# Performance work log

Hardware: AMD Instinct MI355X
Metric: run time of the kernel (lower is better)

## Reference

```python
import jax, jax.numpy as jnp
import numpy as np

N_NODES = 50000
N_EDGES = 800000
N_GRAPHS = 500
IN_DIM, HID, OUT = 128, 64, 10


def setup_inputs() -> dict:
    key = jax.random.key(0)
    ks = jax.random.split(key, 12)
    x = jax.random.normal(ks[0], (N_NODES, IN_DIM), dtype=jnp.float32)
    edge_index = jax.random.randint(ks[1], (2, N_EDGES), 0, N_NODES, dtype=jnp.int32)
    batch = jnp.sort(jax.random.randint(ks[2], (N_NODES,), 0, N_GRAPHS, dtype=jnp.int32))
    def glorot(k, shape):
        lim = np.sqrt(6.0 / (shape[0] + shape[1]))
        return jax.random.uniform(k, shape, jnp.float32, -lim, lim)
    return {
        "x": x, "edge_index": edge_index, "batch": batch,
        "W1": glorot(ks[3], (IN_DIM, HID)), "b1": jnp.zeros((HID,), jnp.float32),
        "W2": glorot(ks[4], (HID, HID)),    "b2": jnp.zeros((HID,), jnp.float32),
        "W3": glorot(ks[5], (HID, HID)),    "b3": jnp.zeros((HID,), jnp.float32),
        "lin_W1": glorot(ks[6], (HID, HID)), "lin_b1": jnp.zeros((HID,), jnp.float32),
        "lin_W2": glorot(ks[7], (HID, OUT)), "lin_b2": jnp.zeros((OUT,), jnp.float32),
    }


def _gcn_conv(x, src, dst, deg_inv_sqrt, W, b):
    # PyG GCNConv: h = x @ W, then sym-normalized scatter-add over edges (self-loops included in src/dst)
    h = x @ W                                   # [N, out]
    norm = deg_inv_sqrt[src] * deg_inv_sqrt[dst]  # [E+N]
    msgs = h[src] * norm[:, None]               # [E+N, out]  (large gathered intermediate)
    out = jax.ops.segment_sum(msgs, dst, num_segments=N_NODES)
    return out + b


def reference(x, edge_index, batch, W1, b1, W2, b2, W3, b3, lin_W1, lin_b1, lin_W2, lin_b2):
    # add self-loops once; degree (with edge weight 1) computed on target nodes
    loops = jnp.arange(N_NODES, dtype=edge_index.dtype)
    src = jnp.concatenate([edge_index[0], loops])
    dst = jnp.concatenate([edge_index[1], loops])
    deg = jax.ops.segment_sum(jnp.ones_like(dst, dtype=x.dtype), dst, num_segments=N_NODES)
    deg_inv_sqrt = jnp.where(deg > 0, jax.lax.rsqrt(jnp.maximum(deg, 1e-12)), 0.0)

    h = jax.nn.relu(_gcn_conv(x, src, dst, deg_inv_sqrt, W1, b1))
    h = jax.nn.relu(_gcn_conv(h, src, dst, deg_inv_sqrt, W2, b2))
    h = jax.nn.relu(_gcn_conv(h, src, dst, deg_inv_sqrt, W3, b3))

    # global mean pool over graphs
    sums = jax.ops.segment_sum(h, batch, num_segments=N_GRAPHS)
    counts = jax.ops.segment_sum(jnp.ones((h.shape[0],), h.dtype), batch, num_segments=N_GRAPHS)
    pooled = sums / jnp.maximum(counts, 1.0)[:, None]  # [G, HID]

    # MLP head (dropout p=0 / eval -> identity)
    logits = jax.nn.relu(pooled @ lin_W1 + lin_b1) @ lin_W2 + lin_b2
    return (logits, jnp.zeros((), x.dtype))
```

## Files before the change

### kernel.cpp

```cpp
#include <hip/hip_runtime.h>
#include <hip/hip_bf16.h>

#define N_NODES 50000
#define N_EDGES 800000
#define N_GRAPHS 500
#define IN_DIM 128
#define HID 64
#define OUT_DIM 10
#define NB_BUCK ((N_NODES + 63) >> 6)
#define NBLK 256
#define BLDT 1024

__device__ __forceinline__ unsigned short f2bf(float f) {
    unsigned x = __float_as_uint(f);
    x += 0x7fffu + ((x >> 16) & 1u);
    return (unsigned short)(x >> 16);
}
__device__ __forceinline__ void acc8(float a[8], uint4 r) {
    a[0] += __uint_as_float(r.x << 16);
    a[1] += __uint_as_float(r.x & 0xffff0000u);
    a[2] += __uint_as_float(r.y << 16);
    a[3] += __uint_as_float(r.y & 0xffff0000u);
    a[4] += __uint_as_float(r.z << 16);
    a[5] += __uint_as_float(r.z & 0xffff0000u);
    a[6] += __uint_as_float(r.w << 16);
    a[7] += __uint_as_float(r.w & 0xffff0000u);
}

__device__ __forceinline__ void gather_node(const unsigned short* __restrict__ hs,
                                            const unsigned short* __restrict__ csr,
                                            int node, int beg, int end, int f8, float a[8]) {
    {
        uint4 u = *(const uint4*)&hs[(size_t)node * 64 + f8];
        acc8(a, u);
    }
    int j = beg;
    for (; j < end && (j & 3); ++j) {
        uint4 r = *(const uint4*)&hs[(size_t)csr[j] * 64 + f8];
        acc8(a, r);
    }
    for (; j + 7 < end; j += 8) {
        ushort4 i0 = *(const ushort4*)&csr[j];
        ushort4 i1 = *(const ushort4*)&csr[j + 4];
        uint4 r0 = *(const uint4*)&hs[(size_t)i0.x * 64 + f8];
        uint4 r1 = *(const uint4*)&hs[(size_t)i0.y * 64 + f8];
        uint4 r2 = *(const uint4*)&hs[(size_t)i0.z * 64 + f8];
        uint4 r3 = *(const uint4*)&hs[(size_t)i0.w * 64 + f8];
        uint4 r4 = *(const uint4*)&hs[(size_t)i1.x * 64 + f8];
        uint4 r5 = *(const uint4*)&hs[(size_t)i1.y * 64 + f8];
        uint4 r6 = *(const uint4*)&hs[(size_t)i1.z * 64 + f8];
        uint4 r7 = *(const uint4*)&hs[(size_t)i1.w * 64 + f8];
        acc8(a, r0); acc8(a, r1); acc8(a, r2); acc8(a, r3);
        acc8(a, r4); acc8(a, r5); acc8(a, r6); acc8(a, r7);
    }
    if (j + 3 < end) {
        ushort4 i0 = *(const ushort4*)&csr[j];
        uint4 r0 = *(const uint4*)&hs[(size_t)i0.x * 64 + f8];
        uint4 r1 = *(const uint4*)&hs[(size_t)i0.y * 64 + f8];
        uint4 r2 = *(const uint4*)&hs[(size_t)i0.z * 64 + f8];
        uint4 r3 = *(const uint4*)&hs[(size_t)i0.w * 64 + f8];
        acc8(a, r0); acc8(a, r1); acc8(a, r2); acc8(a, r3);
        j += 4;
    }
    for (; j < end; ++j) {
        uint4 r = *(const uint4*)&hs[(size_t)csr[j] * 64 + f8];
        acc8(a, r);
    }
}

__global__ __launch_bounds__(BLDT) void p1_hist_kernel(const int* __restrict__ dst,
                                                       int* __restrict__ bhist,
                                                       float* __restrict__ gsum,
                                                       int e, int epb) {
    __shared__ int h[NB_BUCK];
    int tid = threadIdx.x;
    int blk = blockIdx.x;
    {
        int z = blk * BLDT + tid;
        if (z < N_GRAPHS * HID) gsum[z] = 0.0f;
    }
    for (int i = tid; i < NB_BUCK; i += BLDT) h[i] = 0;
    __syncthreads();
    int e0 = blk * epb;
    int e1 = e0 + epb;
    if (e1 > e) e1 = e;
    int i = e0 + tid * 4;
    for (; i + 3 < e1; i += BLDT * 4) {
        int4 d4 = *(const int4*)&dst[i];
        atomicAdd(&h[d4.x >> 6], 1);
        atomicAdd(&h[d4.y >> 6], 1);
        atomicAdd(&h[d4.z >> 6], 1);
        atomicAdd(&h[d4.w >> 6], 1);
    }
    for (int k = i; k < e1 && k < i + 4; ++k) atomicAdd(&h[dst[k] >> 6], 1);
    __syncthreads();
    for (int j = tid; j < NB_BUCK; j += BLDT) bhist[blk * NB_BUCK + j] = h[j];
}

__global__ __launch_bounds__(NBLK) void scanA_kernel(int* __restrict__ bhist,
                                                     int* __restrict__ bsum) {
    __shared__ int s[NBLK];
    int b = blockIdx.x;
    int t = threadIdx.x;
    int c = bhist[t * NB_BUCK + b];
    s[t] = c;
    __syncthreads();
    for (int off = 1; off < NBLK; off <<= 1) {
        int x = (t >= off) ? s[t - off] : 0;
        __syncthreads();
        s[t] += x;
        __syncthreads();
    }
    bhist[t * NB_BUCK + b] = s[t] - c;
    if (t == NBLK - 1) bsum[b] = s[t];
}

__global__ __launch_bounds__(BLDT) void p2_place_kernel(
    const int* __restrict__ src, const int* __restrict__ dst,
    const int* __restrict__ bsum, const int* __restrict__ base,
    unsigned* __restrict__ pairs, int* __restrict__ bstart, int e, int epb) {
    __shared__ int h[NB_BUCK];
    __shared__ int sb[NB_BUCK];
    __shared__ int ts[BLDT];
    int tid = threadIdx.x;
    int blk = blockIdx.x;
    int i0 = tid << 2;
    int v0 = 0, v1 = 0, v2 = 0, v3 = 0;
    if (i0 < NB_BUCK) v0 = bsum[i0];
    if (i0 + 1 < NB_BUCK) v1 = bsum[i0 + 1];
    if (i0 + 2 < NB_BUCK) v2 = bsum[i0 + 2];
    if (i0 + 3 < NB_BUCK) v3 = bsum[i0 + 3];
    int tsum = v0 + v1 + v2 + v3;
    ts[tid] = tsum;
    for (int i = tid; i < NB_BUCK; i += BLDT) h[i] = 0;
    __syncthreads();
    for (int off = 1; off < BLDT; off <<= 1) {
        int x = (tid >= off) ? ts[tid - off] : 0;
        __syncthreads();
        ts[tid] += x;
        __syncthreads();
    }
    int excl = ts[tid] - tsum;
    int s0 = excl;
    int s1 = s0 + v0;
    int s2 = s1 + v1;
    int s3 = s2 + v2;
    const int* bb = base + blk * NB_BUCK;
    if (i0 < NB_BUCK) sb[i0] = s0 + bb[i0];
    if (i0 + 1 < NB_BUCK) sb[i0 + 1] = s1 + bb[i0 + 1];
    if (i0 + 2 < NB_BUCK) sb[i0 + 2] = s2 + bb[i0 + 2];
    if (i0 + 3 < NB_BUCK) sb[i0 + 3] = s3 + bb[i0 + 3];
    if (blk == 0) {
        if (i0 < NB_BUCK) bstart[i0] = s0;
        if (i0 + 1 < NB_BUCK) bstart[i0 + 1] = s1;
        if (i0 + 2 < NB_BUCK) bstart[i0 + 2] = s2;
        if (i0 + 3 < NB_BUCK) bstart[i0 + 3] = s3;
        if (tid == 0) bstart[NB_BUCK] = e;
    }
    __syncthreads();
    int e0 = blk * epb;
    int e1 = e0 + epb;
    if (e1 > e) e1 = e;
    int i = e0 + tid * 4;
    for (; i + 3 < e1; i += BLDT * 4) {
        int4 d4 = *(const int4*)&dst[i];
        int4 s4 = *(const int4*)&src[i];
        int b0 = d4.x >> 6, b1 = d4.y >> 6, b2 = d4.z >> 6, b3 = d4.w >> 6;
        int r0 = atomicAdd(&h[b0], 1);
        int r1 = atomicAdd(&h[b1], 1);
        int r2 = atomicAdd(&h[b2], 1);
        int r3 = atomicAdd(&h[b3], 1);
        pairs[sb[b0] + r0] = ((unsigned)(d4.x & 63) << 16) | (unsigned)s4.x;
        pairs[sb[b1] + r1] = ((unsigned)(d4.y & 63) << 16) | (unsigned)s4.y;
        pairs[sb[b2] + r2] = ((unsigned)(d4.z & 63) << 16) | (unsigned)s4.z;
        pairs[sb[b3] + r3] = ((unsigned)(d4.w & 63) << 16) | (unsigned)s4.w;
    }
    for (int k = i; k < e1 && k < i + 4; ++k) {
        int d = dst[k];
        int b = d >> 6;
        int r = atomicAdd(&h[b], 1);
        pairs[sb[b] + r] = ((unsigned)(d & 63) << 16) | (unsigned)src[k];
    }
}

__global__ __launch_bounds__(256) void csr_lin1_kernel(
    const unsigned* __restrict__ pairs, const int* __restrict__ bstart,
    int* __restrict__ rs, float* __restrict__ dinv, unsigned short* __restrict__ csr_src,
    const float* __restrict__ A, const float* __restrict__ W,
    unsigned short* __restrict__ C, int n) {
    __shared__ float As[64][68];
    __shared__ float Ws[64][64];
    __shared__ int lcnt[64];
    __shared__ int lcur[64];
    __shared__ float sdinv[64];
    int b = blockIdx.x;
    int tid = threadIdx.x;
    int beg = bstart[b], end = bstart[b + 1];
    if (tid < 64) lcnt[tid] = 0;
    __syncthreads();
    for (int i = beg + tid; i < end; i += 256) atomicAdd(&lcnt[pairs[i] >> 16], 1);
    __syncthreads();
    if (tid < 64) {
        int c = lcnt[tid];
        int v = c;
#pragma unroll
        for (int off = 1; off < 64; off <<= 1) {
            int t = __shfl_up(v, off);
            if (tid >= off) v += t;
        }
        int excl = v - c;
        int node = b * 64 + tid;
        float dv = rsqrtf((float)(c + 1));
        if (node <= n) {
            rs[node] = beg + excl;
            if (node < n) dinv[node] = dv;
        }
        sdinv[tid] = dv;
        lcur[tid] = beg + excl;
    }
    __syncthreads();
    for (int i = beg + tid; i < end; i += 256) {
        unsigned p = pairs[i];
        int slot = atomicAdd(&lcur[p >> 16], 1);
        csr_src[slot] = (unsigned short)(p & 0xffffu);
    }

    int block0 = b * 64;
    int rows = n - block0;
    if (rows > 64) rows = 64;
    int tx = tid & 15;
    int ty = tid >> 4;
    float acc[4][4] = {};

    for (int half = 0; half < 2; ++half) {
        __syncthreads();
        {
            const float4* Wv = (const float4*)(W + half * 64 * HID);
            float4* Wsv = (float4*)&Ws[0][0];
            for (int i = tid; i < 64 * 16; i += 256) Wsv[i] = Wv[i];
        }
        for (int idx = tid; idx < 64 * 16; idx += 256) {
            int r = idx >> 4;
            int c4 = (idx & 15) << 2;
            float4 v = {0.f, 0.f, 0.f, 0.f};
            if (r < rows)
                v = *(const float4*)&A[(size_t)(block0 + r) * IN_DIM + half * 64 + c4];
            *(float4*)&As[r][c4] = v;
        }
        __syncthreads();
#pragma unroll 2
        for (int k = 0; k < 64; k += 4) {
            float4 a[4];
#pragma unroll
            for (int i = 0; i < 4; ++i) a[i] = *(const float4*)&As[ty * 4 + i][k];
            float4 w[4];
#pragma unroll
            for (int kk = 0; kk < 4; ++kk) w[kk] = *(const float4*)&Ws[k + kk][tx * 4];
#pragma unroll
            for (int i = 0; i < 4; ++i) {
                float av[4] = {a[i].x, a[i].y, a[i].z, a[i].w};
#pragma unroll
                for (int kk = 0; kk < 4; ++kk) {
                    acc[i][0] += av[kk] * w[kk].x;
                    acc[i][1] += av[kk] * w[kk].y;
                    acc[i][2] += av[kk] * w[kk].z;
                    acc[i][3] += av[kk] * w[kk].w;
                }
            }
        }
    }

#pragma unroll
    for (int i = 0; i < 4; ++i) {
        int r = ty * 4 + i;
        if (r < rows) {
            float s = sdinv[r];
            ushort4 v;
            v.x = f2bf(acc[i][0] * s);
            v.y = f2bf(acc[i][1] * s);
            v.z = f2bf(acc[i][2] * s);
            v.w = f2bf(acc[i][3] * s);
            *(ushort4*)&C[(size_t)(block0 + r) * 64 + tx * 4] = v;
        }
    }
}

__global__ __launch_bounds__(256) void gather_lin_kernel(
    const unsigned short* __restrict__ hs, const int* __restrict__ rs,
    const unsigned short* __restrict__ csr_src, const float* __restrict__ dinv,
    const float* __restrict__ bias, const float* __restrict__ W,
    unsigned short* __restrict__ C, int n) {
    const int K = HID;
    __shared__ float As[32][K + 4];
    __shared__ float Ws[K][64];
    int tid = threadIdx.x;
    int block0 = blockIdx.x * 32;
    int rows = n - block0;
    if (rows > 32) rows = 32;

    {
        const float4* Wv = (const float4*)W;
        float4* Wsv = (float4*)&Ws[0][0];
        for (int i = tid; i < K * 16; i += 256) Wsv[i] = Wv[i];
    }

    int grp = tid >> 3;
    int lg = tid & 7;
    int f8 = lg << 3;
    float4 bb0 = *(const float4*)&bias[f8];
    float4 bb1 = *(const float4*)&bias[f8 + 4];

    int node = block0 + grp;
    float a[8] = {0.f, 0.f, 0.f, 0.f, 0.f, 0.f, 0.f, 0.f};
    if (node < n) {
        int beg = rs[node], end = rs[node + 1];
        gather_node(hs, csr_src, node, beg, end, f8, a);
        float sc = dinv[node];
        a[0] = fmaxf(a[0] * sc + bb0.x, 0.f);
        a[1] = fmaxf(a[1] * sc + bb0.y, 0.f);
        a[2] = fmaxf(a[2] * sc + bb0.z, 0.f);
        a[3] = fmaxf(a[3] * sc + bb0.w, 0.f);
        a[4] = fmaxf(a[4] * sc + bb1.x, 0.f);
        a[5] = fmaxf(a[5] * sc + bb1.y, 0.f);
        a[6] = fmaxf(a[6] * sc + bb1.z, 0.f);
        a[7] = fmaxf(a[7] * sc + bb1.w, 0.f);
    }
    {
        float4 w0 = {a[0], a[1], a[2], a[3]};
        float4 w1 = {a[4], a[5], a[6], a[7]};
        *(float4*)&As[grp][f8] = w0;
        *(float4*)&As[grp][f8 + 4] = w1;
    }
    __syncthreads();

    int tx = tid & 15;
    int ty = tid >> 4;
    float acc[2][4] = {{0.f, 0.f, 0.f, 0.f}, {0.f, 0.f, 0.f, 0.f}};
#pragma unroll 2
    for (int k = 0; k < K; k += 4) {
        float4 aa[2];
#pragma unroll
        for (int i = 0; i < 2; ++i) aa[i] = *(const float4*)&As[ty * 2 + i][k];
        float4 w[4];
#pragma unroll
        for (int kk = 0; kk < 4; ++kk) w[kk] = *(const float4*)&Ws[k + kk][tx * 4];
#pragma unroll
        for (int i = 0; i < 2; ++i) {
            float av[4] = {aa[i].x, aa[i].y, aa[i].z, aa[i].w};
#pragma unroll
            for (int kk = 0; kk < 4; ++kk) {
                acc[i][0] += av[kk] * w[kk].x;
                acc[i][1] += av[kk] * w[kk].y;
                acc[i][2] += av[kk] * w[kk].z;
                acc[i][3] += av[kk] * w[kk].w;
            }
        }
    }

#pragma unroll
    for (int i = 0; i < 2; ++i) {
        int r = ty * 2 + i;
        if (r < rows) {
            float s = dinv[block0 + r];
            ushort4 v;
            v.x = f2bf(acc[i][0] * s);
            v.y = f2bf(acc[i][1] * s);
            v.z = f2bf(acc[i][2] * s);
            v.w = f2bf(acc[i][3] * s);
            *(ushort4*)&C[(size_t)(block0 + r) * 64 + tx * 4] = v;
        }
    }
}

__global__ __launch_bounds__(256) void gather_pool_kernel(
    const unsigned short* __restrict__ hs, const int* __restrict__ rs,
    const unsigned short* __restrict__ csr_src, const float* __restrict__ dinv,
    const float* __restrict__ bias, const int* __restrict__ batch,
    float* __restrict__ gsum, int n) {
    __shared__ float As[32][68];
    int tid = threadIdx.x;
    int block0 = blockIdx.x * 32;
    int rows = n - block0;
    if (rows > 32) rows = 32;

    int grp = tid >> 3;
    int lg = tid & 7;
    int f8 = lg << 3;
    float4 bb0 = *(const float4*)&bias[f8];
    float4 bb1 = *(const float4*)&bias[f8 + 4];

    int node = block0 + grp;
    float a[8] = {0.f, 0.f, 0.f, 0.f, 0.f, 0.f, 0.f, 0.f};
    if (node < n) {
        int beg = rs[node], end = rs[node + 1];
        gather_node(hs, csr_src, node, beg, end, f8, a);
        float sc = dinv[node];
        a[0] = fmaxf(a[0] * sc + bb0.x, 0.f);
        a[1] = fmaxf(a[1] * sc + bb0.y, 0.f);
        a[2] = fmaxf(a[2] * sc + bb0.z, 0.f);
        a[3] = fmaxf(a[3] * sc + bb0.w, 0.f);
        a[4] = fmaxf(a[4] * sc + bb1.x, 0.f);
        a[5] = fmaxf(a[5] * sc + bb1.y, 0.f);
        a[6] = fmaxf(a[6] * sc + bb1.z, 0.f);
        a[7] = fmaxf(a[7] * sc + bb1.w, 0.f);
    }
    {
        float4 w0 = {a[0], a[1], a[2], a[3]};
        float4 w1 = {a[4], a[5], a[6], a[7]};
        *(float4*)&As[grp][f8] = w0;
        *(float4*)&As[grp][f8 + 4] = w1;
    }
    __syncthreads();

    int q = tid >> 6;
    int f = tid & 63;
    int r0 = q * 8;
    int r1 = r0 + 8;
    if (r1 > rows) r1 = rows;
    if (r0 < rows) {
        int gprev = batch[block0 + r0];
        float run = 0.0f;
        for (int r = r0; r < r1; ++r) {
            int g = batch[block0 + r];
            if (g != gprev) {
                atomicAdd(&gsum[(size_t)gprev * 64 + f], run);
                run = 0.0f;
                gprev = g;
            }
            run += As[r][f];
        }
        atomicAdd(&gsum[(size_t)gprev * 64 + f], run);
    }
}

__device__ __forceinline__ int lower_bound_dev(const int* __restrict__ a, int n, int v) {
    int lo = 0, hi = n;
    while (lo < hi) {
        int m = (lo + hi) >> 1;
        if (a[m] < v) lo = m + 1; else hi = m;
    }
    return lo;
}

__global__ __launch_bounds__(64) void head_kernel(
    const float* __restrict__ gsum, const int* __restrict__ batch,
    const float* __restrict__ W1, const float* __restrict__ b1,
    const float* __restrict__ W2, const float* __restrict__ b2,
    float* __restrict__ out, int nNodes, int nGraphs) {
    __shared__ float p[64];
    __shared__ float t64[64];
    int g = blockIdx.x;
    int f = threadIdx.x;
    int lo = lower_bound_dev(batch, nNodes, g);
    int hi = lower_bound_dev(batch, nNodes, g + 1);
    float inv = 1.0f / fmaxf((float)(hi - lo), 1.0f);
    p[f] = gsum[(size_t)g * 64 + f] * inv;
    __syncthreads();
    float acc = b1[f];
#pragma unroll
    for (int k = 0; k < 64; ++k) acc += p[k] * W1[k * 64 + f];
    t64[f] = fmaxf(acc, 0.0f);
    __syncthreads();
    if (f < OUT_DIM) {
        float acc2 = b2[f];
#pragma unroll
        for (int k = 0; k < 64; ++k) acc2 += t64[k] * W2[k * OUT_DIM + f];
        out[g * OUT_DIM + f] = acc2;
    }
    if (g == 0 && f == 0) out[nGraphs * OUT_DIM] = 0.0f;
}

extern "C" void kernel_launch(void* const* d_in, const int* in_sizes, int n_in,
                              void* d_out, int out_size, void* d_ws, size_t ws_size,
                              hipStream_t stream) {
    const float* x      = (const float*)d_in[0];
    const int*   eidx   = (const int*)d_in[1];
    const int*   batch  = (const int*)d_in[2];
    const float* W1     = (const float*)d_in[3];
    const float* b1     = (const float*)d_in[4];
    const float* W2     = (const float*)d_in[5];
    const float* b2     = (const float*)d_in[6];
    const float* W3     = (const float*)d_in[7];
    const float* b3     = (const float*)d_in[8];
    const float* lin_W1 = (const float*)d_in[9];
    const float* lin_b1 = (const float*)d_in[10];
    const float* lin_W2 = (const float*)d_in[11];
    const float* lin_b2 = (const float*)d_in[12];
    float* out = (float*)d_out;

    const int E = in_sizes[1] / 2;
    const int N = N_NODES;
    const int NF = N * HID;
    int epb = (E + NBLK - 1) / NBLK;
    epb = (epb + 7) & ~7;

    const int* src = eidx;
    const int* dst = eidx + E;

    unsigned short* buf1 = (unsigned short*)d_ws;
    unsigned short* buf2 = buf1 + NF;
    float* dinv = (float*)(buf2 + NF);
    int* bhist  = (int*)(dinv + N);
    int* bsum   = bhist + NBLK * NB_BUCK;
    int* bstart = bsum + NB_BUCK;
    int* rs     = bstart + NB_BUCK + 1;
    unsigned short* csr_src =
        (unsigned short*)(((uintptr_t)(rs + N + 1) + 15) & ~(uintptr_t)15);
    unsigned* pairs =
        (unsigned*)(((uintptr_t)(csr_src + E) + 15) & ~(uintptr_t)15);
    float* gsum = (float*)(pairs + E);

    const int TILES = (N + 63) / 64;
    const int G32 = (N + 31) / 32;

    p1_hist_kernel<<<NBLK, BLDT, 0, stream>>>(dst, bhist, gsum, E, epb);
    scanA_kernel<<<NB_BUCK, NBLK, 0, stream>>>(bhist, bsum);
    p2_place_kernel<<<NBLK, BLDT, 0, stream>>>(src, dst, bsum, bhist, pairs, bstart, E, epb);

    csr_lin1_kernel<<<TILES, 256, 0, stream>>>(pairs, bstart, rs, dinv, csr_src,
                                               x, W1, buf1, N);

    gather_lin_kernel<<<G32, 256, 0, stream>>>(buf1, rs, csr_src, dinv, b1, W2, buf2, N);

    gather_lin_kernel<<<G32, 256, 0, stream>>>(buf2, rs, csr_src, dinv, b2, W3, buf1, N);

    gather_pool_kernel<<<G32, 256, 0, stream>>>(buf1, rs, csr_src, dinv, b3, batch, gsum, N);

    head_kernel<<<N_GRAPHS, 64, 0, stream>>>(gsum, batch, lin_W1, lin_b1, lin_W2, lin_b2,
                                             out, N, N_GRAPHS);
}
```

Measured before the change: 215.1 us.

## Split bf16 feature buffers into two half-width planes and gather each half separately

Feature buffers are stored as two planes, the low and high 32 features each in 64-byte rows, and the gather kernels now make two passes, one per plane, with 8-byte loads. Each pass touches a smaller working set, which is meant to improve L2/MALL cache hit rates on random neighbour gathers. CSR index loads switch to scalar nontemporal loads and the bf16 outputs use nontemporal stores. The cost is that the CSR index list is read twice, each row gather issues twice as many smaller loads, and the nontemporal stores may evict data the next layer reads.

```diff
diff --git a/kernel.cpp b/kernel.cpp
--- a/kernel.cpp
+++ b/kernel.cpp
@@ -16,55 +16,70 @@
     x += 0x7fffu + ((x >> 16) & 1u);
     return (unsigned short)(x >> 16);
 }
-__device__ __forceinline__ void acc8(float a[8], uint4 r) {
+__device__ __forceinline__ void acc4(float a[4], uint2 r) {
     a[0] += __uint_as_float(r.x << 16);
     a[1] += __uint_as_float(r.x & 0xffff0000u);
     a[2] += __uint_as_float(r.y << 16);
     a[3] += __uint_as_float(r.y & 0xffff0000u);
-    a[4] += __uint_as_float(r.z << 16);
-    a[5] += __uint_as_float(r.z & 0xffff0000u);
-    a[6] += __uint_as_float(r.w << 16);
-    a[7] += __uint_as_float(r.w & 0xffff0000u);
-}
-
-__device__ __forceinline__ void gather_node(const unsigned short* __restrict__ hs,
+}
+__device__ __forceinline__ unsigned long long pack4(unsigned short x, unsigned short y,
+                                                    unsigned short z, unsigned short w) {
+    return (unsigned long long)x | ((unsigned long long)y << 16) |
+           ((unsigned long long)z << 32) | ((unsigned long long)w << 48);
+}
+
+__device__ __forceinline__ void gather_half(const unsigned short* __restrict__ hsh,
                                             const unsigned short* __restrict__ csr,
-                                            int node, int beg, int end, int f8, float a[8]) {
-    {
-        uint4 u = *(const uint4*)&hs[(size_t)node * 64 + f8];
-        acc8(a, u);
+                                            int node, int beg, int end, int f4, float a[4]) {
+    {
+        uint2 u = *(const uint2*)&hsh[(size_t)node * 32 + f4];
+        acc4(a, u);
     }
     int j = beg;
-    for (; j < end && (j & 3); ++j) {
-        uint4 r = *(const uint4*)&hs[(size_t)csr[j] * 64 + f8];
-        acc8(a, r);
-    }
     for (; j + 7 < end; j += 8) {
-        ushort4 i0 = *(const ushort4*)&csr[j];
-        ushort4 i1 = *(const ushort4*)&csr[j + 4];
-        uint4 r0 = *(const uint4*)&hs[(size_t)i0.x * 64 + f8];
-        uint4 r1 = *(const uint4*)&hs[(size_t)i0.y * 64 + f8];
-        uint4 r2 = *(const uint4*)&hs[(size_t)i0.z * 64 + f8];
-        uint4 r3 = *(const uint4*)&hs[(size_t)i0.w * 64 + f8];
-        uint4 r4 = *(const uint4*)&hs[(size_t)i1.x * 64 + f8];
-        uint4 r5 = *(const uint4*)&hs[(size_t)i1.y * 64 + f8];
-        uint4 r6 = *(const uint4*)&hs[(size_t)i1.z * 64 + f8];
-        uint4 r7 = *(const uint4*)&hs[(size_t)i1.w * 64 + f8];
-        acc8(a, r0); acc8(a, r1); acc8(a, r2); acc8(a, r3);
-        acc8(a, r4); acc8(a, r5); acc8(a, r6); acc8(a, r7);
+        int s0 = (int)__builtin_nontemporal_load(&csr[j]);
+        int s1 = (int)__builtin_nontemporal_load(&csr[j + 1]);
+        int s2 = (int)__builtin_nontemporal_load(&csr[j + 2]);
+        int s3 = (int)__builtin_nontemporal_load(&csr[j + 3]);
+        int s4 = (int)__builtin_nontemporal_load(&csr[j + 4]);
+        int s5 = (int)__builtin_nontemporal_load(&csr[j + 5]);
+        int s6 = (int)__builtin_nontemporal_load(&csr[j + 6]);
+        int s7 = (int)__builtin_nontemporal_load(&csr[j + 7]);
+        uint2 r0 = *(const uint2*)&hsh[(size_t)s0 * 32 + f4];
+        uint2 r1 = *(const uint2*)&hsh[(size_t)s1 * 32 + f4];
+        uint2 r2 = *(const uint2*)&hsh[(size_t)s2 * 32 + f4];
+        uint2 r3 = *(const uint2*)&hsh[(size_t)s3 * 32 + f4];
+        uint2 r4 = *(const uint2*)&hsh[(size_t)s4 * 32 + f4];
+        uint2 r5 = *(const uint2*)&hsh[(size_t)s5 * 32 + f4];
+        uint2 r6 = *(const uint2*)&hsh[(size_t)s6 * 32 + f4];
+        uint2 r7 = *(const uint2*)&hsh[(size_t)s7 * 32 + f4];
+        acc4(a, r0); acc4(a, r1); acc4(a, r2); acc4(a, r3);
+        acc4(a, r4); acc4(a, r5); acc4(a, r6); acc4(a, r7);
     }
     if (j + 3 < end) {
-        ushort4 i0 = *(const ushort4*)&csr[j];
-        uint4 r0 = *(const uint4*)&hs[(size_t)i0.x * 64 + f8];
-        uint4 r1 = *(const uint4*)&hs[(size_t)i0.y * 64 + f8];
-        uint4 r2 = *(const uint4*)&hs[(size_t)i0.z * 64 + f8];
-        uint4 r3 = *(const uint4*)&hs[(size_t)i0.w * 64 + f8];
-        acc8(a, r0); acc8(a, r1); acc8(a, r2); acc8(a, r3);
+        int s0 = (int)__builtin_nontemporal_load(&csr[j]);
+        int s1 = (int)__builtin_nontemporal_load(&csr[j + 1]);
+        int s2 = (int)__builtin_nontemporal_load(&csr[j + 2]);
+        int s3 = (int)__builtin_nontemporal_load(&csr[j + 3]);
+        uint2 r0 = *(const uint2*)&hsh[(size_t)s0 * 32 + f4];
+        uint2 r1 = *(const uint2*)&hsh[(size_t)s1 * 32 + f4];
+        uint2 r2 = *(const uint2*)&hsh[(size_t)s2 * 32 + f4];
+        uint2 r3 = *(const uint2*)&hsh[(size_t)s3 * 32 + f4];
+        acc4(a, r0); acc4(a, r1); acc4(a, r2); acc4(a, r3);
         j += 4;
     }
-    for (; j < end; ++j) {
-        uint4 r = *(const uint4*)&hs[(size_t)csr[j] * 64 + f8];
-        acc8(a, r);
+    if (j + 1 < end) {
+        int s0 = (int)__builtin_nontemporal_load(&csr[j]);
+        int s1 = (int)__builtin_nontemporal_load(&csr[j + 1]);
+        uint2 r0 = *(const uint2*)&hsh[(size_t)s0 * 32 + f4];
+        uint2 r1 = *(const uint2*)&hsh[(size_t)s1 * 32 + f4];
+        acc4(a, r0); acc4(a, r1);
+        j += 2;
+    }
+    if (j < end) {
+        int s0 = (int)__builtin_nontemporal_load(&csr[j]);
+        uint2 r0 = *(const uint2*)&hsh[(size_t)s0 * 32 + f4];
+        acc4(a, r0);
     }
 }
 
@@ -187,7 +202,7 @@
     const unsigned* __restrict__ pairs, const int* __restrict__ bstart,
     int* __restrict__ rs, float* __restrict__ dinv, unsigned short* __restrict__ csr_src,
     const float* __restrict__ A, const float* __restrict__ W,
-    unsigned short* __restrict__ C, int n) {
+    unsigned short* __restrict__ C_lo, unsigned short* __restrict__ C_hi, int n) {
     __shared__ float As[64][68];
     __shared__ float Ws[64][64];
     __shared__ int lcnt[64];
@@ -275,21 +290,22 @@
         int r = ty * 4 + i;
         if (r < rows) {
             float s = sdinv[r];
-            ushort4 v;
-            v.x = f2bf(acc[i][0] * s);
-            v.y = f2bf(acc[i][1] * s);
-            v.z = f2bf(acc[i][2] * s);
-            v.w = f2bf(acc[i][3] * s);
-            *(ushort4*)&C[(size_t)(block0 + r) * 64 + tx * 4] = v;
+            unsigned long long pk = pack4(f2bf(acc[i][0] * s), f2bf(acc[i][1] * s),
+                                          f2bf(acc[i][2] * s), f2bf(acc[i][3] * s));
+            unsigned short* p = (tx < 8)
+                ? &C_lo[(size_t)(block0 + r) * 32 + tx * 4]
+                : &C_hi[(size_t)(block0 + r) * 32 + (tx - 8) * 4];
+            __builtin_nontemporal_store(pk, (unsigned long long*)p);
         }
     }
 }
 
 __global__ __launch_bounds__(256) void gather_lin_kernel(
-    const unsigned short* __restrict__ hs, const int* __restrict__ rs,
-    const unsigned short* __restrict__ csr_src, const float* __restrict__ dinv,
-    const float* __restrict__ bias, const float* __restrict__ W,
-    unsigned short* __restrict__ C, int n) {
+    const unsigned short* __restrict__ hs_lo, const unsigned short* __restrict__ hs_hi,
+    const int* __restrict__ rs, const unsigned short* __restrict__ csr_src,
+    const float* __restrict__ dinv, const float* __restrict__ bias,
+    const float* __restrict__ W, unsigned short* __restrict__ C_lo,
+    unsigned short* __restrict__ C_hi, int n) {
     const int K = HID;
     __shared__ float As[32][K + 4];
     __shared__ float Ws[K][64];
@@ -306,30 +322,41 @@
 
     int grp = tid >> 3;
     int lg = tid & 7;
-    int f8 = lg << 3;
-    float4 bb0 = *(const float4*)&bias[f8];
-    float4 bb1 = *(const float4*)&bias[f8 + 4];
-
+    int f4 = lg << 2;
     int node = block0 + grp;
-    float a[8] = {0.f, 0.f, 0.f, 0.f, 0.f, 0.f, 0.f, 0.f};
+    int beg = 0, end = 0;
+    float sc = 0.f;
     if (node < n) {
-        int beg = rs[node], end = rs[node + 1];
-        gather_node(hs, csr_src, node, beg, end, f8, a);
-        float sc = dinv[node];
-        a[0] = fmaxf(a[0] * sc + bb0.x, 0.f);
-        a[1] = fmaxf(a[1] * sc + bb0.y, 0.f);
-        a[2] = fmaxf(a[2] * sc + bb0.z, 0.f);
-        a[3] = fmaxf(a[3] * sc + bb0.w, 0.f);
-        a[4] = fmaxf(a[4] * sc + bb1.x, 0.f);
-        a[5] = fmaxf(a[5] * sc + bb1.y, 0.f);
-        a[6] = fmaxf(a[6] * sc + bb1.z, 0.f);
-        a[7] = fmaxf(a[7] * sc + bb1.w, 0.f);
-    }
-    {
+        beg = rs[node];
+        end = rs[node + 1];
+        sc = dinv[node];
+    }
+
+    {
+        float a[4] = {0.f, 0.f, 0.f, 0.f};
+        if (node < n) {
+            gather_half(hs_lo, csr_src, node, beg, end, f4, a);
+            float4 bb = *(const float4*)&bias[f4];
+            a[0] = fmaxf(a[0] * sc + bb.x, 0.f);
+            a[1] = fmaxf(a[1] * sc + bb.y, 0.f);
+            a[2] = fmaxf(a[2] * sc + bb.z, 0.f);
+            a[3] = fmaxf(a[3] * sc + bb.w, 0.f);
+        }
         float4 w0 = {a[0], a[1], a[2], a[3]};
-        float4 w1 = {a[4], a[5], a[6], a[7]};
-        *(float4*)&As[grp][f8] = w0;
-        *(float4*)&As[grp][f8 + 4] = w1;
+        *(float4*)&As[grp][f4] = w0;
+    }
+    {
+        float a[4] = {0.f, 0.f, 0.f, 0.f};
+        if (node < n) {
+            gather_half(hs_hi, csr_src, node, beg, end, f4, a);
+            float4 bb = *(const float4*)&bias[32 + f4];
+            a[0] = fmaxf(a[0] * sc + bb.x, 0.f);
+            a[1] = fmaxf(a[1] * sc + bb.y, 0.f);
+            a[2] = fmaxf(a[2] * sc + bb.z, 0.f);
+            a[3] = fmaxf(a[3] * sc + bb.w, 0.f);
+        }
+        float4 w1 = {a[0], a[1], a[2], a[3]};
+        *(float4*)&As[grp][32 + f4] = w1;
     }
     __syncthreads();
 
@@ -362,21 +389,21 @@
         int r = ty * 2 + i;
         if (r < rows) {
             float s = dinv[block0 + r];
-            ushort4 v;
-            v.x = f2bf(acc[i][0] * s);
-            v.y = f2bf(acc[i][1] * s);
-            v.z = f2bf(acc[i][2] * s);
-            v.w = f2bf(acc[i][3] * s);
-            *(ushort4*)&C[(size_t)(block0 + r) * 64 + tx * 4] = v;
+            unsigned long long pk = pack4(f2bf(acc[i][0] * s), f2bf(acc[i][1] * s),
+                                          f2bf(acc[i][2] * s), f2bf(acc[i][3] * s));
+            unsigned short* p = (tx < 8)
+                ? &C_lo[(size_t)(block0 + r) * 32 + tx * 4]
+                : &C_hi[(size_t)(block0 + r) * 32 + (tx - 8) * 4];
+            __builtin_nontemporal_store(pk, (unsigned long long*)p);
         }
     }
 }
 
 __global__ __launch_bounds__(256) void gather_pool_kernel(
-    const unsigned short* __restrict__ hs, const int* __restrict__ rs,
-    const unsigned short* __restrict__ csr_src, const float* __restrict__ dinv,
-    const float* __restrict__ bias, const int* __restrict__ batch,
-    float* __restrict__ gsum, int n) {
+    const unsigned short* __restrict__ hs_lo, const unsigned short* __restrict__ hs_hi,
+    const int* __restrict__ rs, const unsigned short* __restrict__ csr_src,
+    const float* __restrict__ dinv, const float* __restrict__ bias,
+    const int* __restrict__ batch, float* __restrict__ gsum, int n) {
     __shared__ float As[32][68];
     int tid = threadIdx.x;
     int block0 = blockIdx.x * 32;
@@ -385,30 +412,41 @@
 
     int grp = tid >> 3;
     int lg = tid & 7;
-    int f8 = lg << 3;
-    float4 bb0 = *(const float4*)&bias[f8];
-    float4 bb1 = *(const float4*)&bias[f8 + 4];
-
+    int f4 = lg << 2;
     int node = block0 + grp;
-    float a[8] = {0.f, 0.f, 0.f, 0.f, 0.f, 0.f, 0.f, 0.f};
+    int beg = 0, end = 0;
+    float sc = 0.f;
     if (node < n) {
-        int beg = rs[node], end = rs[node + 1];
-        gather_node(hs, csr_src, node, beg, end, f8, a);
-        float sc = dinv[node];
-        a[0] = fmaxf(a[0] * sc + bb0.x, 0.f);
-        a[1] = fmaxf(a[1] * sc + bb0.y, 0.f);
-        a[2] = fmaxf(a[2] * sc + bb0.z, 0.f);
-        a[3] = fmaxf(a[3] * sc + bb0.w, 0.f);
-        a[4] = fmaxf(a[4] * sc + bb1.x, 0.f);
-        a[5] = fmaxf(a[5] * sc + bb1.y, 0.f);
-        a[6] = fmaxf(a[6] * sc + bb1.z, 0.f);
-        a[7] = fmaxf(a[7] * sc + bb1.w, 0.f);
-    }
-    {
+        beg = rs[node];
+        end = rs[node + 1];
+        sc = dinv[node];
+    }
+
+    {
+        float a[4] = {0.f, 0.f, 0.f, 0.f};
+        if (node < n) {
+            gather_half(hs_lo, csr_src, node, beg, end, f4, a);
+            float4 bb = *(const float4*)&bias[f4];
+            a[0] = fmaxf(a[0] * sc + bb.x, 0.f);
+            a[1] = fmaxf(a[1] * sc + bb.y, 0.f);
+            a[2] = fmaxf(a[2] * sc + bb.z, 0.f);
+            a[3] = fmaxf(a[3] * sc + bb.w, 0.f);
+        }
         float4 w0 = {a[0], a[1], a[2], a[3]};
-        float4 w1 = {a[4], a[5], a[6], a[7]};
-        *(float4*)&As[grp][f8] = w0;
-        *(float4*)&As[grp][f8 + 4] = w1;
+        *(float4*)&As[grp][f4] = w0;
+    }
+    {
+        float a[4] = {0.f, 0.f, 0.f, 0.f};
+        if (node < n) {
+            gather_half(hs_hi, csr_src, node, beg, end, f4, a);
+            float4 bb = *(const float4*)&bias[32 + f4];
+            a[0] = fmaxf(a[0] * sc + bb.x, 0.f);
+            a[1] = fmaxf(a[1] * sc + bb.y, 0.f);
+            a[2] = fmaxf(a[2] * sc + bb.z, 0.f);
+            a[3] = fmaxf(a[3] * sc + bb.w, 0.f);
+        }
+        float4 w1 = {a[0], a[1], a[2], a[3]};
+        *(float4*)&As[grp][32 + f4] = w1;
     }
     __syncthreads();
 
@@ -498,7 +536,11 @@
     const int* dst = eidx + E;
 
     unsigned short* buf1 = (unsigned short*)d_ws;
+    unsigned short* buf1_lo = buf1;
+    unsigned short* buf1_hi = buf1 + (size_t)N * 32;
     unsigned short* buf2 = buf1 + NF;
+    unsigned short* buf2_lo = buf2;
+    unsigned short* buf2_hi = buf2 + (size_t)N * 32;
     float* dinv = (float*)(buf2 + NF);
     int* bhist  = (int*)(dinv + N);
     int* bsum   = bhist + NBLK * NB_BUCK;
@@ -518,13 +560,16 @@
     p2_place_kernel<<<NBLK, BLDT, 0, stream>>>(src, dst, bsum, bhist, pairs, bstart, E, epb);
 
     csr_lin1_kernel<<<TILES, 256, 0, stream>>>(pairs, bstart, rs, dinv, csr_src,
-                                               x, W1, buf1, N);
-
-    gather_lin_kernel<<<G32, 256, 0, stream>>>(buf1, rs, csr_src, dinv, b1, W2, buf2, N);
-
-    gather_lin_kernel<<<G32, 256, 0, stream>>>(buf2, rs, csr_src, dinv, b2, W3, buf1, N);
-
-    gather_pool_kernel<<<G32, 256, 0, stream>>>(buf1, rs, csr_src, dinv, b3, batch, gsum, N);
+                                               x, W1, buf1_lo, buf1_hi, N);
+
+    gather_lin_kernel<<<G32, 256, 0, stream>>>(buf1_lo, buf1_hi, rs, csr_src, dinv,
+                                               b1, W2, buf2_lo, buf2_hi, N);
+
+    gather_lin_kernel<<<G32, 256, 0, stream>>>(buf2_lo, buf2_hi, rs, csr_src, dinv,
+                                               b2, W3, buf1_lo, buf1_hi, N);
+
+    gather_pool_kernel<<<G32, 256, 0, stream>>>(buf1_lo, buf1_hi, rs, csr_src, dinv,
+                                                b3, batch, gsum, N);
 
     head_kernel<<<N_GRAPHS, 64, 0, stream>>>(gsum, batch, lin_W1, lin_b1, lin_W2, lin_b2,
                                              out, N, N_GRAPHS);
```

New measurement: 234.1 us. +8.8%, slower.
